# Kernel optimization log

Measured on AMD Instinct MI355X. Metric: run time of the kernel, lower is better.

## Reference

```python
import jax, jax.numpy as jnp
from jax import lax
import numpy as np

INPUT_SIZE, HIDDEN, NUM_LAYERS = 64, 512, 2
BATCH, SEQ = 256, 512


def setup_inputs() -> dict:
    key = jax.random.key(0)
    ks = jax.random.split(key, 16)
    k_lim = 1.0 / np.sqrt(HIDDEN)  # torch LSTMCell init range
    u = lambda k, shape: jax.random.uniform(k, shape, jnp.float32, -k_lim, k_lim)
    inp = {"x": jax.random.normal(ks[0], (BATCH, SEQ, INPUT_SIZE), jnp.float32)}
    for layer in range(NUM_LAYERS):
        in_size = INPUT_SIZE if layer == 0 else HIDDEN
        base = 1 + 4 * layer
        inp[f"W_ih{layer}"] = u(ks[base + 0], (4 * HIDDEN, in_size))
        inp[f"W_hh{layer}"] = u(ks[base + 1], (4 * HIDDEN, HIDDEN))
        inp[f"b_ih{layer}"] = u(ks[base + 2], (4 * HIDDEN,))
        inp[f"b_hh{layer}"] = u(ks[base + 3], (4 * HIDDEN,))
    inp["fc_w"] = u(ks[10], (1, HIDDEN))
    inp["fc_b"] = u(ks[11], (1,))
    return inp


def _lstm_layer(xs, W_ih, W_hh, b_ih, b_hh):
    """xs: [T, B, in] -> (hs [T, B, H], h_last [B, H])."""
    H = W_hh.shape[1]
    B = xs.shape[1]
    # Input projection for all timesteps at once (one big GEMM).
    pre = jnp.einsum('tbi,gi->tbg', xs, W_ih) + b_ih + b_hh  # [T, B, 4H]

    def step(carry, p):
        h, c = carry
        gates = p + h @ W_hh.T  # [B, 4H], gate order i,f,g,o
        i, f, g, o = jnp.split(gates, 4, axis=-1)
        i, f, o = jax.nn.sigmoid(i), jax.nn.sigmoid(f), jax.nn.sigmoid(o)
        c = f * c + i * jnp.tanh(g)
        h = o * jnp.tanh(c)
        return (h, c), h

    init = (jnp.zeros((B, H), xs.dtype), jnp.zeros((B, H), xs.dtype))
    (h_last, _), hs = lax.scan(step, init, pre)
    return hs, h_last


def reference(x, W_ih0, W_hh0, b_ih0, b_hh0, W_ih1, W_hh1, b_ih1, b_hh1, fc_w, fc_b):
    params = [(W_ih0, W_hh0, b_ih0, b_hh0), (W_ih1, W_hh1, b_ih1, b_hh1)]
    xs = jnp.transpose(x, (1, 0, 2))  # [T, B, in]
    h_last = None
    for (W_ih, W_hh, b_ih, b_hh) in params:
        xs, h_last = _lstm_layer(xs, W_ih, W_hh, b_ih, b_hh)
    # dropout p=0.0 / eval mode -> identity
    return (h_last @ fc_w.T + fc_b)[:, 0]  # [B]
```

## Files before the change

kernel.cpp:

```cpp
#include <hip/hip_runtime.h>
#include <math.h>

#define T_SEQ 512
#define BATCH 256
#define HID   512
#define IN0   64
#define K1    1024
#define K0    576
#define NWG   256
#define NTHR  256
#define LDS_DYN 131072

typedef _Float16 f16x8 __attribute__((ext_vector_type(8)));
typedef float    f32x4 __attribute__((ext_vector_type(4)));

__device__ __forceinline__ float sigm(float x)   { return 1.0f / (1.0f + __expf(-x)); }
__device__ __forceinline__ float tanh_f(float x) { return 2.0f / (1.0f + __expf(-2.0f * x)) - 1.0f; }

__device__ __forceinline__ f32x4 mfma16(f16x8 a, f16x8 b, f32x4 c) {
  return __builtin_amdgcn_mfma_f32_16x16x32_f16(a, b, c, 0, 0, 0);
}

__device__ __forceinline__ f16x8 load_f16x8_cc(const _Float16* p) {
  f16x8 r;
  asm volatile("global_load_dwordx4 %0, %1, off sc0 sc1"
               : "=v"(r) : "v"((const void*)p));
  return r;
}
__device__ __forceinline__ void store_short_wt(const _Float16* p, unsigned v) {
  asm volatile("global_store_short %0, %1, off sc0 sc1"
               :: "v"((const void*)p), "v"(v) : "memory");
}
__device__ __forceinline__ void store_dword_wt(const unsigned* p, unsigned v) {
  asm volatile("global_store_dword %0, %1, off sc0 sc1"
               :: "v"((const void*)p), "v"(v) : "memory");
}

__global__ void k_split_w(const float* __restrict__ Wih, const float* __restrict__ Whh,
                          const float* __restrict__ bih, const float* __restrict__ bhh,
                          _Float16* __restrict__ whi, float* __restrict__ bias, int Kin) {
  int K = Kin + HID;
  long idx = (long)blockIdx.x * 256 + threadIdx.x;
  long total = 2048L * K;
  if (idx < total) {
    int k = (int)(idx % K);
    int r = (int)(idx / K);
    int gate = r & 3, hcol = r >> 2;
    int row = gate * HID + hcol;
    float v = (k < Kin) ? Wih[(long)row * Kin + k] : Whh[(long)row * HID + (k - Kin)];
    long o = (long)(r >> 4) * 16 * K + (long)(k >> 3) * 128 + (r & 15) * 8 + (k & 7);
    whi[o] = (_Float16)v;
  }
  if (idx < 2048) {
    int r = (int)idx;
    int gate = r & 3, hcol = r >> 2;
    int row = gate * HID + hcol;
    bias[r] = bih[row] + bhh[row];
  }
}

__global__ void k_split_x(const float* __restrict__ x, _Float16* __restrict__ x16) {
  int idx = blockIdx.x * 256 + threadIdx.x;
  int i = idx & 63;
  int b = (idx >> 6) & 255;
  int t = idx >> 14;
  x16[idx] = (_Float16)x[((size_t)b * T_SEQ + t) * IN0 + i];
}

__device__ __forceinline__ void grid_barrier(unsigned* bar, unsigned epoch, unsigned dom) {
  __syncthreads();
  if (threadIdx.x == 0) {
    unsigned a = __hip_atomic_fetch_add(&bar[dom * 32], 1u,
                                        __ATOMIC_RELAXED, __HIP_MEMORY_SCOPE_AGENT);
    if (a == epoch * 64u - 1u)
      store_dword_wt(&bar[256 + dom * 32], epoch);
    while ((int)(__hip_atomic_load(&bar[256 + dom * 32],
                                   __ATOMIC_RELAXED, __HIP_MEMORY_SCOPE_AGENT) - epoch) < 0)
      __builtin_amdgcn_s_sleep(4);
  }
  __syncthreads();
}

__global__ __launch_bounds__(NTHR, 1) void k_lstm(
    const _Float16* __restrict__ x16,
    const _Float16* __restrict__ w0, const float* __restrict__ bias0,
    const _Float16* __restrict__ w1, const float* __restrict__ bias1,
    _Float16* __restrict__ in1,
    const float* __restrict__ fcw, const float* __restrict__ fcb,
    float* __restrict__ out, unsigned* __restrict__ bar)
{
  extern __shared__ __align__(16) _Float16 ldsA[];

  const int tid  = threadIdx.x;
  const int lane = tid & 63;
  const int wv   = __builtin_amdgcn_readfirstlane(tid >> 6);
  const int wg   = blockIdx.x;
  const int layer1 = (wg < 128) ? 1 : 0;
  const int lw   = wg & 127;
  const int rg   = lw >> 2;
  const int bg   = lw & 3;
  const unsigned dom = (unsigned)bg;
  const int bbase = bg * 64 + wv * 16;
  const int lr = lane & 15;
  const int lg = lane >> 4;
  const int KW = layer1 ? K1 : K0;

  {
    const f16x8* gw = reinterpret_cast<const f16x8*>((layer1 ? w1 : w0) + (size_t)rg * 64 * KW);
    f16x8* lw16 = reinterpret_cast<f16x8*>(ldsA);
    const int nch = 8 * KW;
    for (int ch = tid; ch < nch; ch += NTHR) lw16[ch] = gw[ch];
  }
  __syncthreads();

  const float* bsrc = layer1 ? bias1 : bias0;
  float4 b4[4];
  int hcv[4];
  #pragma unroll
  for (int sl = 0; sl < 4; ++sl) {
    hcv[sl] = rg * 16 + sl * 4 + lg;
    b4[sl] = *reinterpret_cast<const float4*>(bsrc + hcv[sl] * 4);
  }
  const f16x8* A = reinterpret_cast<const f16x8*>(ldsA);

  float c[4] = {0.f, 0.f, 0.f, 0.f};

  #pragma unroll 1
  for (int n = 0; n <= T_SEQ; ++n) {
    const int pr = (n + 1) & 1;
    const int pw = n & 1;
    const bool active = layer1 ? (n >= 1) : (n < T_SEQ);
    if (active) {
      f32x4 acc[4];
      #pragma unroll
      for (int sl = 0; sl < 4; ++sl) {
        acc[sl][0]=b4[sl].x; acc[sl][1]=b4[sl].y; acc[sl][2]=b4[sl].z; acc[sl][3]=b4[sl].w;
      }

      const _Float16* Bp = in1 + ((size_t)pr * BATCH + bbase) * K1 + (size_t)lr * K1 + lg * 8;

      if (layer1) {
        f16x8 bufA[16], bufB[16];
        #pragma unroll
        for (int kk = 0; kk < 16; ++kk)
          bufA[kk] = load_f16x8_cc(Bp + (size_t)kk * 32);
        #pragma unroll
        for (int kk = 0; kk < 16; ++kk)
          bufB[kk] = load_f16x8_cc(Bp + (size_t)(16 + kk) * 32);
        asm volatile("s_waitcnt vmcnt(16)" ::: "memory");
        __builtin_amdgcn_sched_barrier(0);
        #pragma unroll
        for (int kk = 0; kk < 16; ++kk) {
          const int ac = (kk * 4 + lg) * 16 + lr;
          #pragma unroll
          for (int sl = 0; sl < 4; ++sl)
            acc[sl] = mfma16(A[(size_t)sl * 2 * K1 + ac], bufA[kk], acc[sl]);
        }
        asm volatile("s_waitcnt vmcnt(0)" ::: "memory");
        __builtin_amdgcn_sched_barrier(0);
        #pragma unroll
        for (int kk = 0; kk < 16; ++kk) {
          const int ac = ((16 + kk) * 4 + lg) * 16 + lr;
          #pragma unroll
          for (int sl = 0; sl < 4; ++sl)
            acc[sl] = mfma16(A[(size_t)sl * 2 * K1 + ac], bufB[kk], acc[sl]);
        }
      } else {
        const _Float16* Xp = x16 + ((size_t)n * BATCH + bbase) * IN0 + (size_t)lr * IN0 + lg * 8;
        f16x8 xb0 = load_f16x8_cc(Xp);
        f16x8 xb1 = load_f16x8_cc(Xp + 32);
        f16x8 bufA[16];
        #pragma unroll
        for (int kk = 0; kk < 16; ++kk)
          bufA[kk] = load_f16x8_cc(Bp + (size_t)kk * 32);
        asm volatile("s_waitcnt vmcnt(16)" ::: "memory");
        __builtin_amdgcn_sched_barrier(0);
        #pragma unroll
        for (int sl = 0; sl < 4; ++sl)
          acc[sl] = mfma16(A[(size_t)sl * 2 * K0 + (lg * 16 + lr)], xb0, acc[sl]);
        #pragma unroll
        for (int sl = 0; sl < 4; ++sl)
          acc[sl] = mfma16(A[(size_t)sl * 2 * K0 + ((4 + lg) * 16 + lr)], xb1, acc[sl]);
        asm volatile("s_waitcnt vmcnt(0)" ::: "memory");
        __builtin_amdgcn_sched_barrier(0);
        #pragma unroll
        for (int kk = 0; kk < 16; ++kk) {
          const int ac = (8 + kk * 4 + lg) * 16 + lr;
          #pragma unroll
          for (int sl = 0; sl < 4; ++sl)
            acc[sl] = mfma16(A[(size_t)sl * 2 * K0 + ac], bufA[kk], acc[sl]);
        }
      }

      const int b = bbase + lr;
      #pragma unroll
      for (int sl = 0; sl < 4; ++sl) {
        float i_ = sigm(acc[sl][0]);
        float f_ = sigm(acc[sl][1]);
        float g_ = tanh_f(acc[sl][2]);
        float o_ = sigm(acc[sl][3]);
        c[sl] = fmaf(f_, c[sl], i_ * g_);
        float hv = o_ * tanh_f(c[sl]);
        _Float16 h16 = (_Float16)hv;
        const int col = (layer1 ? 512 : 0) + hcv[sl];
        const size_t idx = ((size_t)pw * BATCH + b) * K1 + col;
        store_short_wt(in1 + idx, (unsigned)__builtin_bit_cast(unsigned short, h16));
      }
      asm volatile("s_waitcnt vmcnt(0)" ::: "memory");
    }
    grid_barrier(bar, (unsigned)(n + 1), dom);
  }

  if (wg == 0) {
    if (tid == 0) {
      #pragma unroll
      for (int d = 0; d < 4; ++d)
        while ((int)(__hip_atomic_load(&bar[256 + d * 32],
                                       __ATOMIC_RELAXED, __HIP_MEMORY_SCOPE_AGENT)
                     - (unsigned)(T_SEQ + 1)) < 0)
          __builtin_amdgcn_s_sleep(4);
      __builtin_amdgcn_fence(__ATOMIC_ACQUIRE, "agent");
    }
    __syncthreads();
    if (tid < BATCH) {
      const _Float16* r = in1 + (size_t)tid * K1 + 512;
      float acc = 0.f;
      #pragma unroll 8
      for (int k = 0; k < HID; ++k)
        acc = fmaf((float)r[k], fcw[k], acc);
      out[tid] = acc + fcb[0];
    }
  }
}

extern "C" void kernel_launch(void* const* d_in, const int* in_sizes, int n_in,
                              void* d_out, int out_size, void* d_ws, size_t ws_size,
                              hipStream_t stream) {
  const float* x    = (const float*)d_in[0];
  const float* Wih0 = (const float*)d_in[1];
  const float* Whh0 = (const float*)d_in[2];
  const float* bih0 = (const float*)d_in[3];
  const float* bhh0 = (const float*)d_in[4];
  const float* Wih1 = (const float*)d_in[5];
  const float* Whh1 = (const float*)d_in[6];
  const float* bih1 = (const float*)d_in[7];
  const float* bhh1 = (const float*)d_in[8];
  const float* fcw  = (const float*)d_in[9];
  const float* fcb  = (const float*)d_in[10];

  char* ws = (char*)d_ws;
  size_t off = 0;
  auto alloc = [&](size_t bytes) -> char* {
    char* pp = ws + off;
    off = (off + bytes + 1023) & ~(size_t)1023;
    return pp;
  };
  unsigned*  bar  = (unsigned*)alloc(4096);
  _Float16* x16  = (_Float16*)alloc((size_t)T_SEQ * BATCH * IN0 * 2);
  _Float16* w0   = (_Float16*)alloc((size_t)2048 * K0 * 2);
  _Float16* w1   = (_Float16*)alloc((size_t)2048 * K1 * 2);
  float*    bias0 = (float*)alloc(2048 * 4);
  float*    bias1 = (float*)alloc(2048 * 4);
  _Float16* in1  = (_Float16*)alloc((size_t)2 * BATCH * K1 * 2);

  (void)hipFuncSetAttribute(reinterpret_cast<const void*>(k_lstm),
                            hipFuncAttributeMaxDynamicSharedMemorySize, LDS_DYN);

  (void)hipMemsetAsync(bar, 0, 4096, stream);
  (void)hipMemsetAsync(in1, 0, (size_t)2 * BATCH * K1 * 2, stream);
  k_split_x<<<(T_SEQ * BATCH * IN0) / 256, 256, 0, stream>>>(x, x16);
  k_split_w<<<(int)((2048L * K0 + 255) / 256), 256, 0, stream>>>(Wih0, Whh0, bih0, bhh0, w0, bias0, IN0);
  k_split_w<<<(int)((2048L * K1 + 255) / 256), 256, 0, stream>>>(Wih1, Whh1, bih1, bhh1, w1, bias1, HID);
  k_lstm<<<NWG, NTHR, LDS_DYN, stream>>>(x16, w0, bias0, w1, bias1,
                                         in1, fcw, fcb, (float*)d_out, bar);
}
```

Measured before the change: 4.328 ms.

## Replace per-step grid barrier with split read/write dataflow counters per domain

```diff
diff --git a/kernel.cpp b/kernel.cpp
--- a/kernel.cpp
+++ b/kernel.cpp
@@ -34,6 +34,14 @@
 __device__ __forceinline__ void store_dword_wt(const unsigned* p, unsigned v) {
   asm volatile("global_store_dword %0, %1, off sc0 sc1"
                :: "v"((const void*)p), "v"(v) : "memory");
+}
+
+__device__ __forceinline__ unsigned sig_add(unsigned* p) {
+  return __hip_atomic_fetch_add(p, 1u, __ATOMIC_RELAXED, __HIP_MEMORY_SCOPE_AGENT);
+}
+__device__ __forceinline__ void sig_wait(const unsigned* p, unsigned tgt) {
+  while ((int)(__hip_atomic_load(p, __ATOMIC_RELAXED, __HIP_MEMORY_SCOPE_AGENT) - tgt) < 0)
+    __builtin_amdgcn_s_sleep(4);
 }
 
 __global__ void k_split_w(const float* __restrict__ Wih, const float* __restrict__ Whh,
@@ -67,20 +75,6 @@
   x16[idx] = (_Float16)x[((size_t)b * T_SEQ + t) * IN0 + i];
 }
 
-__device__ __forceinline__ void grid_barrier(unsigned* bar, unsigned epoch, unsigned dom) {
-  __syncthreads();
-  if (threadIdx.x == 0) {
-    unsigned a = __hip_atomic_fetch_add(&bar[dom * 32], 1u,
-                                        __ATOMIC_RELAXED, __HIP_MEMORY_SCOPE_AGENT);
-    if (a == epoch * 64u - 1u)
-      store_dword_wt(&bar[256 + dom * 32], epoch);
-    while ((int)(__hip_atomic_load(&bar[256 + dom * 32],
-                                   __ATOMIC_RELAXED, __HIP_MEMORY_SCOPE_AGENT) - epoch) < 0)
-      __builtin_amdgcn_s_sleep(4);
-  }
-  __syncthreads();
-}
-
 __global__ __launch_bounds__(NTHR, 1) void k_lstm(
     const _Float16* __restrict__ x16,
     const _Float16* __restrict__ w0, const float* __restrict__ bias0,
@@ -105,6 +99,15 @@
   const int lg = lane >> 4;
   const int KW = layer1 ? K1 : K0;
 
+  unsigned* RD0c = bar + 0   + dom * 32;
+  unsigned* RD0r = bar + 128 + dom * 32;
+  unsigned* RD1c = bar + 256 + dom * 32;
+  unsigned* RD1r = bar + 384 + dom * 32;
+  unsigned* W0c  = bar + 512 + dom * 32;
+  unsigned* W0r  = bar + 640 + dom * 32;
+  unsigned* W1c  = bar + 768 + dom * 32;
+  unsigned* W1r  = bar + 896 + dom * 32;
+
   {
     const f16x8* gw = reinterpret_cast<const f16x8*>((layer1 ? w1 : w0) + (size_t)rg * 64 * KW);
     f16x8* lw16 = reinterpret_cast<f16x8*>(ldsA);
@@ -140,10 +143,14 @@
       const _Float16* Bp = in1 + ((size_t)pr * BATCH + bbase) * K1 + (size_t)lr * K1 + lg * 8;
 
       if (layer1) {
+        if (tid == 0) sig_wait(W0r, 32u * (unsigned)n);
+        __syncthreads();
         f16x8 bufA[16], bufB[16];
         #pragma unroll
         for (int kk = 0; kk < 16; ++kk)
           bufA[kk] = load_f16x8_cc(Bp + (size_t)kk * 32);
+        if (tid == 0) sig_wait(W1r, 32u * (unsigned)(n - 1));
+        __syncthreads();
         #pragma unroll
         for (int kk = 0; kk < 16; ++kk)
           bufB[kk] = load_f16x8_cc(Bp + (size_t)(16 + kk) * 32);
@@ -158,6 +165,11 @@
         }
         asm volatile("s_waitcnt vmcnt(0)" ::: "memory");
         __builtin_amdgcn_sched_barrier(0);
+        __syncthreads();
+        if (tid == 0) {
+          unsigned a = sig_add(RD1c);
+          if (a == 32u * (unsigned)n - 1u) store_dword_wt(RD1r, 32u * (unsigned)n);
+        }
         #pragma unroll
         for (int kk = 0; kk < 16; ++kk) {
           const int ac = ((16 + kk) * 4 + lg) * 16 + lr;
@@ -169,6 +181,8 @@
         const _Float16* Xp = x16 + ((size_t)n * BATCH + bbase) * IN0 + (size_t)lr * IN0 + lg * 8;
         f16x8 xb0 = load_f16x8_cc(Xp);
         f16x8 xb1 = load_f16x8_cc(Xp + 32);
+        if (tid == 0 && n > 0) sig_wait(W0r, 32u * (unsigned)n);
+        __syncthreads();
         f16x8 bufA[16];
         #pragma unroll
         for (int kk = 0; kk < 16; ++kk)
@@ -183,6 +197,11 @@
           acc[sl] = mfma16(A[(size_t)sl * 2 * K0 + ((4 + lg) * 16 + lr)], xb1, acc[sl]);
         asm volatile("s_waitcnt vmcnt(0)" ::: "memory");
         __builtin_amdgcn_sched_barrier(0);
+        __syncthreads();
+        if (tid == 0) {
+          unsigned a = sig_add(RD0c);
+          if (a == 32u * (unsigned)(n + 1) - 1u) store_dword_wt(RD0r, 32u * (unsigned)(n + 1));
+        }
         #pragma unroll
         for (int kk = 0; kk < 16; ++kk) {
           const int ac = (8 + kk * 4 + lg) * 16 + lr;
@@ -191,6 +210,12 @@
             acc[sl] = mfma16(A[(size_t)sl * 2 * K0 + ac], bufA[kk], acc[sl]);
         }
       }
+
+      if (tid == 0 && n >= 1) {
+        sig_wait(RD0r, 32u * (unsigned)n);
+        sig_wait(RD1r, 32u * (unsigned)(n - 1));
+      }
+      __syncthreads();
 
       const int b = bbase + lr;
       #pragma unroll
@@ -207,18 +232,24 @@
         store_short_wt(in1 + idx, (unsigned)__builtin_bit_cast(unsigned short, h16));
       }
       asm volatile("s_waitcnt vmcnt(0)" ::: "memory");
+      __syncthreads();
+      if (tid == 0) {
+        if (layer1) {
+          unsigned a = sig_add(W1c);
+          if (a == 32u * (unsigned)n - 1u) store_dword_wt(W1r, 32u * (unsigned)n);
+        } else {
+          unsigned a = sig_add(W0c);
+          if (a == 32u * (unsigned)(n + 1) - 1u) store_dword_wt(W0r, 32u * (unsigned)(n + 1));
+        }
+      }
     }
-    grid_barrier(bar, (unsigned)(n + 1), dom);
   }
 
   if (wg == 0) {
     if (tid == 0) {
       #pragma unroll
       for (int d = 0; d < 4; ++d)
-        while ((int)(__hip_atomic_load(&bar[256 + d * 32],
-                                       __ATOMIC_RELAXED, __HIP_MEMORY_SCOPE_AGENT)
-                     - (unsigned)(T_SEQ + 1)) < 0)
-          __builtin_amdgcn_s_sleep(4);
+        sig_wait(bar + 896 + d * 32, 32u * (unsigned)T_SEQ);
       __builtin_amdgcn_fence(__ATOMIC_ACQUIRE, "agent");
     }
     __syncthreads();
```

Measured after the change: 4.591 ms. 1.06x slower.
